# Optimization experiments

Hardware: AMD Instinct MI355X
Metric: run time of the kernel (lower is better)

## Reference

```python
import jax, jax.numpy as jnp
import numpy as np

B, N, DIM, H, DH = 16, 1024, 768, 12, 64
SCALE = DH ** -0.5


def setup_inputs() -> dict:
    key = jax.random.key(0)
    k1, k2, k3 = jax.random.split(key, 3)
    x = jax.random.normal(k1, (B, N, DIM), dtype=jnp.float32)
    W_qkv = jax.random.normal(k2, (DIM, 3 * H * DH), dtype=jnp.float32) * (DIM ** -0.5)
    W_out = jax.random.normal(k3, (H * DH, DIM), dtype=jnp.float32) * ((H * DH) ** -0.5)
    b_out = jnp.zeros((DIM,), dtype=jnp.float32)
    # perm = [0] + random shuffle of 1..N-1 (matches module's construction)
    rng = np.random.default_rng(0)
    perm = jnp.asarray(np.concatenate([[0], rng.permutation(np.arange(1, N))]), dtype=jnp.int32)
    return {"x": x, "W_qkv": W_qkv, "W_out": W_out, "b_out": b_out, "perm": perm}


def reference(x, W_qkv, W_out, b_out, perm):
    # QKV projection: [b, n, 3*h*d]
    qkv = jnp.einsum('bnd,de->bne', x, W_qkv)
    q, k, v = jnp.split(qkv, 3, axis=-1)
    # [b, n, h*d] -> [b, h, n, d]
    reshape = lambda t: t.reshape(B, N, H, DH).transpose(0, 2, 1, 3)
    q, k, v = reshape(q), reshape(k), reshape(v)
    # permute query rows
    q = q[:, :, perm]
    dots = jnp.einsum('bhqd,bhkd->bhqk', q, k) * SCALE
    attn = jax.nn.softmax(dots, axis=-1)
    out = jnp.einsum('bhqk,bhkd->bhqd', attn, v)
    out = out.transpose(0, 2, 1, 3).reshape(B, N, H * DH)
    return jnp.einsum('bne,ed->bnd', out, W_out) + b_out
```

## Files before the change

### kernel.cpp

```cpp
#include <hip/hip_runtime.h>
#include <hip/hip_bf16.h>


typedef __bf16 bf16x8 __attribute__((ext_vector_type(8)));
typedef __bf16 bf16x4 __attribute__((ext_vector_type(4)));
typedef float  f32x4  __attribute__((ext_vector_type(4)));

__device__ __forceinline__ f32x4 mfma16(bf16x8 a, bf16x8 b, f32x4 c) {
    return __builtin_amdgcn_mfma_f32_16x16x32_bf16(a, b, c, 0, 0, 0);
}

__device__ __forceinline__ void async16(const void* g, void* l) {
    __builtin_amdgcn_global_load_lds(
        (const __attribute__((address_space(1))) unsigned int*)g,
        (__attribute__((address_space(3))) unsigned int*)l,
        16, 0, 0);
}

__global__ void detect_dtype(const unsigned short* __restrict__ raw, int* __restrict__ flag) {
    __shared__ int cnt;
    if (threadIdx.x == 0) cnt = 0;
    __syncthreads();
    int local = 0;
    for (int i = threadIdx.x; i < 2048; i += 256) {
        unsigned e = (raw[i] >> 7) & 0xFFu;
        if (e >= 0xC0u) local++;
    }
    atomicAdd(&cnt, local);
    __syncthreads();
    if (threadIdx.x == 0) *flag = (cnt > 16) ? 1 : 0;
}

__global__ void convert_to_bf16(const void* __restrict__ src, __bf16* __restrict__ dst,
                                int n4, const int* __restrict__ flag) {
    const int f = *flag;
    int i = blockIdx.x * blockDim.x + threadIdx.x;
    const int stride = gridDim.x * blockDim.x;
    if (f) {
        const float4* s = (const float4*)src;
        for (; i < n4; i += stride) {
            float4 v = s[i];
            bf16x4 o;
            o[0] = (__bf16)v.x; o[1] = (__bf16)v.y;
            o[2] = (__bf16)v.z; o[3] = (__bf16)v.w;
            *(bf16x4*)&dst[(size_t)i * 4] = o;
        }
    } else {
        const ushort4* s = (const ushort4*)src;
        for (; i < n4; i += stride) *(ushort4*)&dst[(size_t)i * 4] = s[i];
    }
}

__global__ void transpose_dyn(const void* __restrict__ in, __bf16* __restrict__ out,
                              int R, int C, const int* __restrict__ flag) {
    __shared__ __bf16 tile[64][65];
    const int f = *flag;
    const int c0 = blockIdx.x * 64, r0 = blockIdx.y * 64;
    const int tx = threadIdx.x, ty = threadIdx.y;
#pragma unroll
    for (int k = 0; k < 16; ++k) {
        int r = ty + 4 * k;
        size_t idx = (size_t)(r0 + r) * C + c0 + tx;
        tile[r][tx] = f ? (__bf16)((const float*)in)[idx] : ((const __bf16*)in)[idx];
    }
    __syncthreads();
#pragma unroll
    for (int k = 0; k < 16; ++k) {
        int cc = ty + 4 * k;
        out[(size_t)(c0 + cc) * R + r0 + tx] = tile[tx][cc];
    }
}

__global__ void transpose_v(const __bf16* __restrict__ qkv, __bf16* __restrict__ vt) {
    __shared__ __bf16 tile[64][65];
    const int bh = blockIdx.y;
    const int b = bh / 12, h = bh % 12;
    const int n0 = blockIdx.x * 64;
    const int tx = threadIdx.x, ty = threadIdx.y;
#pragma unroll
    for (int k = 0; k < 16; ++k) {
        int n = ty + 4 * k;
        tile[n][tx] = qkv[((size_t)b * 1024 + n0 + n) * 2304 + 1536 + h * 64 + tx];
    }
    __syncthreads();
#pragma unroll
    for (int k = 0; k < 16; ++k) {
        int d = ty + 4 * k;
        vt[((size_t)bh * 64 + d) * 1024 + n0 + tx] = tile[tx][d];
    }
}

template <int MODE>
__global__ __launch_bounds__(256)
void gemm_bt(const __bf16* __restrict__ A, int lda,
             const __bf16* __restrict__ Bt,
             const void* __restrict__ bias,
             void* __restrict__ Cout, int ldc,
             int K, const int* __restrict__ flag) {
    __shared__ __align__(16) char smem[16384];
    __bf16* lsA = (__bf16*)smem;
    __bf16* lsB = (__bf16*)(smem + 8192);
    const int tid  = threadIdx.x;
    const int wid  = tid >> 6;
    const int lane = tid & 63;
    const int quad = lane >> 4;
    const int l15  = lane & 15;
    const int bm = blockIdx.x * 128;
    const int bn = blockIdx.y * 128;
    const int wm = (wid & 1) * 64;
    const int wn = (wid >> 1) * 64;
    const int srow  = lane >> 2;
    const int sslot = lane & 3;

    f32x4 acc[4][4];
#pragma unroll
    for (int i = 0; i < 4; ++i)
#pragma unroll
        for (int j = 0; j < 4; ++j) acc[i][j] = (f32x4)0.0f;

    for (int k0 = 0; k0 < K; k0 += 32) {
        __syncthreads();
#pragma unroll
        for (int is = 0; is < 2; ++is) {
            int r  = is * 64 + wid * 16 + srow;
            int gc = k0 + ((sslot ^ ((r >> 1) & 3)) << 3);
            async16(A + (size_t)(bm + r) * lda + gc, &lsA[(is * 64 + wid * 16) * 32]);
        }
#pragma unroll
        for (int is = 0; is < 2; ++is) {
            int r  = is * 64 + wid * 16 + srow;
            int gc = k0 + ((sslot ^ ((r >> 1) & 3)) << 3);
            async16(Bt + (size_t)(bn + r) * K + gc, &lsB[(is * 64 + wid * 16) * 32]);
        }
        __syncthreads();

        bf16x8 af[4], bfr[4];
#pragma unroll
        for (int mi = 0; mi < 4; ++mi) {
            int r = wm + mi * 16 + l15;
            af[mi] = *(const bf16x8*)&lsA[r * 32 + (quad ^ ((r >> 1) & 3)) * 8];
        }
#pragma unroll
        for (int ni = 0; ni < 4; ++ni) {
            int r = wn + ni * 16 + l15;
            bfr[ni] = *(const bf16x8*)&lsB[r * 32 + (quad ^ ((r >> 1) & 3)) * 8];
        }
#pragma unroll
        for (int mi = 0; mi < 4; ++mi)
#pragma unroll
            for (int ni = 0; ni < 4; ++ni)
                acc[mi][ni] = mfma16(af[mi], bfr[ni], acc[mi][ni]);
    }

    const int f = (MODE == 1) ? *flag : 0;
    if (MODE == 1) {
#pragma unroll
        for (int ni = 0; ni < 4; ++ni) {
            int col = bn + wn + ni * 16 + l15;
            float bv = f ? ((const float*)bias)[col] : (float)((const __bf16*)bias)[col];
#pragma unroll
            for (int mi = 0; mi < 4; ++mi)
#pragma unroll
                for (int rg = 0; rg < 4; ++rg) acc[mi][ni][rg] += bv;
        }
    }

    if (MODE == 0 || !f) {
        __bf16* cs = (__bf16*)smem;
#pragma unroll
        for (int c = 0; c < 4; ++c) {
            __syncthreads();
            if (wm == (c >> 1) * 64) {
                int mb = (c & 1) * 2;
#pragma unroll
                for (int mloc = 0; mloc < 2; ++mloc) {
                    int rowc = mloc * 16 + quad * 4;
#pragma unroll
                    for (int ni = 0; ni < 4; ++ni) {
                        int col = wn + ni * 16 + l15;
#pragma unroll
                        for (int rg = 0; rg < 4; ++rg)
                            cs[(rowc + rg) * 136 + col] = (__bf16)acc[mb + mloc][ni][rg];
                    }
                }
            }
            __syncthreads();
#pragma unroll
            for (int p = 0; p < 2; ++p) {
                int row  = p * 16 + (tid >> 4);
                int colc = tid & 15;
                bf16x8 v = *(const bf16x8*)&cs[row * 136 + colc * 8];
                *(bf16x8*)((__bf16*)Cout + (size_t)(bm + c * 32 + row) * ldc + bn + colc * 8) = v;
            }
        }
    } else {
        float* cs = (float*)smem;
#pragma unroll
        for (int c = 0; c < 8; ++c) {
            __syncthreads();
            if (wm == (c >> 2) * 64) {
                int mi = c & 3;
                int rowc = quad * 4;
#pragma unroll
                for (int ni = 0; ni < 4; ++ni) {
                    int col = wn + ni * 16 + l15;
#pragma unroll
                    for (int rg = 0; rg < 4; ++rg)
                        cs[(rowc + rg) * 132 + col] = acc[mi][ni][rg];
                }
            }
            __syncthreads();
#pragma unroll
            for (int p = 0; p < 2; ++p) {
                int row  = p * 8 + (tid >> 5);
                int colc = tid & 31;
                float4 v = *(const float4*)&cs[row * 132 + colc * 4];
                *(float4*)((float*)Cout + (size_t)(bm + c * 16 + row) * ldc + bn + colc * 4) = v;
            }
        }
    }
}

__global__ __launch_bounds__(256, 2)
void attn(const __bf16* qkv, const __bf16* __restrict__ vt,
          const int* __restrict__ perm, __bf16* O, int ldo) {
    __shared__ __align__(16) char smem[38912];
    __bf16* Qs = (__bf16*)smem;
    __bf16* Ks = (__bf16*)smem;
    __bf16* Vs = (__bf16*)(smem + 8192);
    __bf16* Ps = (__bf16*)(smem + 16384);

    const int tid  = threadIdx.x;
    const int wid  = tid >> 6;
    const int lane = tid & 63;
    const int quad = lane >> 4;
    const int l15  = lane & 15;
    const int bh = blockIdx.x;
    const int q0 = blockIdx.y * 128;
    const int b = bh / 12, h = bh % 12;
    const size_t row_base = (size_t)b * 1024;
    const int qcol = h * 64;
    const int kcol = 768 + h * 64;
    const int srow8  = lane >> 3;
    const int sslot8 = lane & 7;
    __bf16* Pw = Ps + wid * (32 * 88);

#pragma unroll
    for (int is = 0; is < 4; ++is) {
        int r = is * 32 + wid * 8 + srow8;
        int gr = perm[q0 + r];
        int chunk = sslot8 ^ (r & 7);
        async16(qkv + (row_base + gr) * 2304 + qcol + chunk * 8,
                &Qs[(is * 32 + wid * 8) * 64]);
    }
    __syncthreads();

    bf16x8 qf[2][2];
#pragma unroll
    for (int mi = 0; mi < 2; ++mi) {
        int r = wid * 32 + mi * 16 + l15;
#pragma unroll
        for (int ks = 0; ks < 2; ++ks)
            qf[mi][ks] = *(const bf16x8*)&Qs[r * 64 + (((ks * 4 + quad) ^ (r & 7)) * 8)];
    }

    const int off0 = l15 * 64 + (((0 * 4 + quad) ^ (l15 & 7)) * 8);
    const int off1 = l15 * 64 + (((1 * 4 + quad) ^ (l15 & 7)) * 8);
    const int pwb  = l15 * 88 + quad * 4;
    const int pfb  = l15 * 88 + quad * 8;

    const int rK = wid * 8 + srow8;
    const int ck = sslot8 ^ (rK & 7);
    const __bf16* kg0 = qkv + (row_base + rK) * 2304 + kcol + ck * 8;
    const __bf16* kg1 = kg0 + (size_t)32 * 2304;
    const __bf16* vg0 = vt + ((size_t)bh * 64 + rK) * 1024 + ck * 8;
    const __bf16* vg1 = vg0 + (size_t)32 * 1024;

    f32x4 acco[2][4];
#pragma unroll
    for (int mi = 0; mi < 2; ++mi)
#pragma unroll
        for (int ni = 0; ni < 4; ++ni) acco[mi][ni] = (f32x4)0.0f;
    float lsum[2] = {0.0f, 0.0f};

    const float cfac = 0.125f * 1.44269504088896340736f;

    for (int kt = 0; kt < 16; ++kt) {
        __syncthreads();
        async16(kg0, &Ks[(wid * 8) * 64]);
        async16(kg1, &Ks[(32 + wid * 8) * 64]);
        async16(vg0, &Vs[(wid * 8) * 64]);
        async16(vg1, &Vs[(32 + wid * 8) * 64]);
        kg0 += (size_t)64 * 2304;
        kg1 += (size_t)64 * 2304;
        vg0 += 64;
        vg1 += 64;
        __syncthreads();

#pragma unroll
        for (int half = 0; half < 2; ++half) {
            f32x4 accs[2][2];
#pragma unroll
            for (int ki = 0; ki < 2; ++ki)
#pragma unroll
                for (int mi = 0; mi < 2; ++mi) accs[ki][mi] = (f32x4)0.0f;
#pragma unroll
            for (int ks = 0; ks < 2; ++ks) {
                const int off = ks ? off1 : off0;
                bf16x8 kf0 = *(const bf16x8*)&Ks[(half * 2 + 0) * 1024 + off];
                bf16x8 kf1 = *(const bf16x8*)&Ks[(half * 2 + 1) * 1024 + off];
                accs[0][0] = mfma16(kf0, qf[0][ks], accs[0][0]);
                accs[0][1] = mfma16(kf0, qf[1][ks], accs[0][1]);
                accs[1][0] = mfma16(kf1, qf[0][ks], accs[1][0]);
                accs[1][1] = mfma16(kf1, qf[1][ks], accs[1][1]);
            }

#pragma unroll
            for (int ki = 0; ki < 2; ++ki)
#pragma unroll
                for (int mi = 0; mi < 2; ++mi) {
                    bf16x4 pk;
                    float s0 = __builtin_amdgcn_exp2f(accs[ki][mi][0] * cfac - 8.0f);
                    float s1 = __builtin_amdgcn_exp2f(accs[ki][mi][1] * cfac - 8.0f);
                    float s2 = __builtin_amdgcn_exp2f(accs[ki][mi][2] * cfac - 8.0f);
                    float s3 = __builtin_amdgcn_exp2f(accs[ki][mi][3] * cfac - 8.0f);
                    pk[0] = (__bf16)s0; pk[1] = (__bf16)s1;
                    pk[2] = (__bf16)s2; pk[3] = (__bf16)s3;
                    lsum[mi] += (s0 + s1) + (s2 + s3);
                    *(bf16x4*)&Pw[pwb + mi * 1408 + (half * 2 + ki) * 16] = pk;
                }

            {
                bf16x8 pf0 = *(const bf16x8*)&Pw[pfb + 0 * 1408 + half * 32];
                bf16x8 pf1 = *(const bf16x8*)&Pw[pfb + 1 * 1408 + half * 32];
                const int offv = half ? off1 : off0;
#pragma unroll
                for (int ni = 0; ni < 4; ++ni) {
                    bf16x8 vf = *(const bf16x8*)&Vs[ni * 1024 + offv];
                    acco[0][ni] = mfma16(pf0, vf, acco[0][ni]);
                    acco[1][ni] = mfma16(pf1, vf, acco[1][ni]);
                }
            }
        }
    }

#pragma unroll
    for (int off = 16; off < 64; off <<= 1) {
        lsum[0] += __shfl_xor(lsum[0], off, 64);
        lsum[1] += __shfl_xor(lsum[1], off, 64);
    }

#pragma unroll
    for (int mi = 0; mi < 2; ++mi) {
#pragma unroll
        for (int rg = 0; rg < 4; ++rg) {
            float inv = 1.0f / __shfl(lsum[mi], quad * 4 + rg, 64);
            int orow = q0 + wid * 32 + mi * 16 + quad * 4 + rg;
#pragma unroll
            for (int ni = 0; ni < 4; ++ni) {
                int ocol = h * 64 + ni * 16 + l15;
                O[(row_base + orow) * (size_t)ldo + ocol] = (__bf16)(acco[mi][ni][rg] * inv);
            }
        }
    }
}

extern "C" void kernel_launch(void* const* d_in, const int* in_sizes, int n_in,
                              void* d_out, int out_size, void* d_ws, size_t ws_size,
                              hipStream_t stream) {
    (void)in_sizes; (void)n_in; (void)out_size; (void)ws_size;
    const void* x_raw    = d_in[0];
    const void* Wqkv_raw = d_in[1];
    const void* Wout_raw = d_in[2];
    const void* bout_raw = d_in[3];
    const int*  perm     = (const int*)d_in[4];

    char* ws = (char*)d_ws;
    int*    flag = (int*)ws;
    __bf16* Xc   = (__bf16*)(ws + 256);
    __bf16* QKV  = (__bf16*)(ws + 25166080);
    __bf16* Vt   = (__bf16*)(ws + 100663552);
    __bf16* Wqt  = (__bf16*)(ws + 125829376);
    __bf16* Wot  = (__bf16*)(ws + 129368320);
    __bf16* Obuf = QKV + 1536;

    detect_dtype<<<1, 256, 0, stream>>>((const unsigned short*)x_raw, flag);
    convert_to_bf16<<<2048, 256, 0, stream>>>(x_raw, Xc, 16384 * 768 / 4, flag);
    transpose_dyn<<<dim3(36, 12), dim3(64, 4), 0, stream>>>(Wqkv_raw, Wqt, 768, 2304, flag);
    transpose_dyn<<<dim3(12, 12), dim3(64, 4), 0, stream>>>(Wout_raw, Wot, 768, 768, flag);
    gemm_bt<0><<<dim3(128, 18), 256, 0, stream>>>(Xc, 768, Wqt, nullptr, QKV, 2304, 768, nullptr);
    transpose_v<<<dim3(16, 192), dim3(64, 4), 0, stream>>>(QKV, Vt);
    attn<<<dim3(192, 8), 256, 0, stream>>>(QKV, Vt, perm, Obuf, 2304);
    gemm_bt<1><<<dim3(128, 6), 256, 0, stream>>>(Obuf, 2304, Wot, bout_raw, d_out, 768, 768, flag);
}
```

Measured before the change: 227.3 us.

## Use 256x256-tile double-buffered GEMM kernel for QKV projection

```diff
diff --git a/kernel.cpp b/kernel.cpp
--- a/kernel.cpp
+++ b/kernel.cpp
@@ -87,6 +87,181 @@
     for (int k = 0; k < 16; ++k) {
         int d = ty + 4 * k;
         vt[((size_t)bh * 64 + d) * 1024 + n0 + tx] = tile[tx][d];
+    }
+}
+
+__global__ __launch_bounds__(512, 2)
+void gemm256_bt(const __bf16* __restrict__ A, int lda,
+                const __bf16* __restrict__ Bt, int ldb,
+                __bf16* __restrict__ Cout, int ldc, int K) {
+    __shared__ __align__(16) char smem[131072];
+    const int tid  = threadIdx.x;
+    const int wid  = tid >> 6;
+    const int lane = tid & 63;
+    const int quad = lane >> 4;
+    const int l15  = lane & 15;
+    const int wr   = wid >> 2;
+    const int wc   = wid & 3;
+    const int bm = blockIdx.x * 256;
+    const int bn = blockIdx.y * 256;
+    const int srow8  = lane >> 3;
+    const int sslot8 = lane & 7;
+
+    const int offk[2] = { l15 * 128 + (((quad    ) ^ (l15 & 7)) * 16),
+                          l15 * 128 + (((quad | 4) ^ (l15 & 7)) * 16) };
+
+    const int cchunk = (sslot8 ^ srow8) * 8;
+    const __bf16* gA[4];
+    const __bf16* gB[4];
+#pragma unroll
+    for (int p = 0; p < 4; ++p) {
+        int r = (wid * 4 + p) * 8 + srow8;
+        gA[p] = A  + (size_t)(bm + r) * lda + cchunk;
+        gB[p] = Bt + (size_t)(bn + r) * ldb + cchunk;
+    }
+
+    f32x4 acc[8][4];
+#pragma unroll
+    for (int i = 0; i < 8; ++i)
+#pragma unroll
+        for (int j = 0; j < 4; ++j) acc[i][j] = (f32x4)0.0f;
+
+#pragma unroll
+    for (int p = 0; p < 4; ++p) {
+        async16(gA[p], smem + (wid * 4 + p) * 1024);
+        async16(gB[p], smem + 65536 + (wid * 4 + p) * 1024);
+        gA[p] += 64; gB[p] += 64;
+    }
+    asm volatile("s_waitcnt vmcnt(0)" ::: "memory");
+    __builtin_amdgcn_s_barrier();
+
+    const int nkt = K >> 6;
+    int cur = 0;
+#pragma unroll 1
+    for (int kt = 0; kt < nkt; ++kt) {
+        const bool notlast = (kt != nkt - 1);
+        const char* aRd = smem + cur + wr * 16384;
+        const char* bRd = smem + 65536 + cur + wc * 8192;
+        char* aSt = smem + (cur ^ 32768);
+        char* bSt = smem + 65536 + (cur ^ 32768);
+        bf16x8 af[4][2], bfr[4][2];
+
+#pragma unroll
+        for (int i = 0; i < 4; ++i)
+#pragma unroll
+            for (int kk = 0; kk < 2; ++kk)
+                af[i][kk] = *(const bf16x8*)(aRd + offk[kk] + i * 2048);
+#pragma unroll
+        for (int j = 0; j < 2; ++j)
+#pragma unroll
+            for (int kk = 0; kk < 2; ++kk)
+                bfr[j][kk] = *(const bf16x8*)(bRd + offk[kk] + j * 2048);
+        if (notlast) {
+#pragma unroll
+            for (int p = 0; p < 4; ++p) {
+                async16(gA[p], aSt + (wid * 4 + p) * 1024);
+                gA[p] += 64;
+            }
+        }
+        __builtin_amdgcn_s_barrier();
+        asm volatile("s_waitcnt lgkmcnt(0)" ::: "memory");
+        __builtin_amdgcn_sched_barrier(0);
+        __builtin_amdgcn_s_setprio(1);
+#pragma unroll
+        for (int i = 0; i < 4; ++i)
+#pragma unroll
+            for (int j = 0; j < 2; ++j)
+#pragma unroll
+                for (int kk = 0; kk < 2; ++kk)
+                    acc[i][j] = mfma16(af[i][kk], bfr[j][kk], acc[i][j]);
+        __builtin_amdgcn_s_setprio(0);
+        __builtin_amdgcn_s_barrier();
+
+#pragma unroll
+        for (int j = 0; j < 2; ++j)
+#pragma unroll
+            for (int kk = 0; kk < 2; ++kk)
+                bfr[2 + j][kk] = *(const bf16x8*)(bRd + offk[kk] + (2 + j) * 2048);
+        if (notlast) {
+#pragma unroll
+            for (int p = 0; p < 4; ++p) {
+                async16(gB[p], bSt + (wid * 4 + p) * 1024);
+                gB[p] += 64;
+            }
+        }
+        __builtin_amdgcn_s_barrier();
+        asm volatile("s_waitcnt lgkmcnt(0)" ::: "memory");
+        __builtin_amdgcn_sched_barrier(0);
+        __builtin_amdgcn_s_setprio(1);
+#pragma unroll
+        for (int i = 0; i < 4; ++i)
+#pragma unroll
+            for (int j = 0; j < 2; ++j)
+#pragma unroll
+                for (int kk = 0; kk < 2; ++kk)
+                    acc[i][2 + j] = mfma16(af[i][kk], bfr[2 + j][kk], acc[i][2 + j]);
+        __builtin_amdgcn_s_setprio(0);
+        __builtin_amdgcn_s_barrier();
+
+#pragma unroll
+        for (int i = 0; i < 4; ++i)
+#pragma unroll
+            for (int kk = 0; kk < 2; ++kk)
+                af[i][kk] = *(const bf16x8*)(aRd + offk[kk] + (4 + i) * 2048);
+        __builtin_amdgcn_s_barrier();
+        asm volatile("s_waitcnt lgkmcnt(0)" ::: "memory");
+        __builtin_amdgcn_sched_barrier(0);
+        __builtin_amdgcn_s_setprio(1);
+#pragma unroll
+        for (int i = 0; i < 4; ++i)
+#pragma unroll
+            for (int j = 0; j < 2; ++j)
+#pragma unroll
+                for (int kk = 0; kk < 2; ++kk)
+                    acc[4 + i][j] = mfma16(af[i][kk], bfr[j][kk], acc[4 + i][j]);
+        __builtin_amdgcn_s_setprio(0);
+        __builtin_amdgcn_s_barrier();
+
+        __builtin_amdgcn_s_setprio(1);
+#pragma unroll
+        for (int i = 0; i < 4; ++i)
+#pragma unroll
+            for (int j = 0; j < 2; ++j)
+#pragma unroll
+                for (int kk = 0; kk < 2; ++kk)
+                    acc[4 + i][2 + j] = mfma16(af[i][kk], bfr[2 + j][kk], acc[4 + i][2 + j]);
+        __builtin_amdgcn_s_setprio(0);
+        asm volatile("s_waitcnt vmcnt(0)" ::: "memory");
+        __builtin_amdgcn_s_barrier();
+        cur ^= 32768;
+    }
+
+    __bf16* cs = (__bf16*)smem;
+#pragma unroll 1
+    for (int c = 0; c < 8; ++c) {
+        __syncthreads();
+        if (wr == (c >> 2)) {
+            int mbase = (c & 3) * 2;
+#pragma unroll
+            for (int mloc = 0; mloc < 2; ++mloc) {
+#pragma unroll
+                for (int ni = 0; ni < 4; ++ni) {
+                    int col = wc * 64 + ni * 16 + l15;
+#pragma unroll
+                    for (int rg = 0; rg < 4; ++rg)
+                        cs[(mloc * 16 + quad * 4 + rg) * 264 + col] =
+                            (__bf16)acc[mbase + mloc][ni][rg];
+                }
+            }
+        }
+        __syncthreads();
+#pragma unroll
+        for (int p = 0; p < 2; ++p) {
+            int row  = p * 16 + (tid >> 5);
+            int colc = tid & 31;
+            bf16x8 v = *(const bf16x8*)&cs[row * 264 + colc * 8];
+            *(bf16x8*)&Cout[(size_t)(bm + c * 32 + row) * ldc + bn + colc * 8] = v;
+        }
     }
 }
 
@@ -388,7 +563,7 @@
     convert_to_bf16<<<2048, 256, 0, stream>>>(x_raw, Xc, 16384 * 768 / 4, flag);
     transpose_dyn<<<dim3(36, 12), dim3(64, 4), 0, stream>>>(Wqkv_raw, Wqt, 768, 2304, flag);
     transpose_dyn<<<dim3(12, 12), dim3(64, 4), 0, stream>>>(Wout_raw, Wot, 768, 768, flag);
-    gemm_bt<0><<<dim3(128, 18), 256, 0, stream>>>(Xc, 768, Wqt, nullptr, QKV, 2304, 768, nullptr);
+    gemm256_bt<<<dim3(64, 9), 512, 0, stream>>>(Xc, 768, Wqt, 768, QKV, 2304, 768);
     transpose_v<<<dim3(16, 192), dim3(64, 4), 0, stream>>>(QKV, Vt);
     attn<<<dim3(192, 8), 256, 0, stream>>>(QKV, Vt, perm, Obuf, 2304);
     gemm_bt<1><<<dim3(128, 6), 256, 0, stream>>>(Obuf, 2304, Wot, bout_raw, d_out, 768, 768, flag);
```

Result: slower. 308.4 us (+35.7%).

## Add 256x256 triple-buffered GEMM kernel for the QKV projection

Applied to the files above, without the earlier changes.

```diff
diff --git a/kernel.cpp b/kernel.cpp
--- a/kernel.cpp
+++ b/kernel.cpp
@@ -87,6 +87,132 @@
     for (int k = 0; k < 16; ++k) {
         int d = ty + 4 * k;
         vt[((size_t)bh * 64 + d) * 1024 + n0 + tx] = tile[tx][d];
+    }
+}
+
+#define MF4(I, AV) \
+    acc[I][0] = mfma16(AV, b0, acc[I][0]); \
+    acc[I][1] = mfma16(AV, b1, acc[I][1]); \
+    acc[I][2] = mfma16(AV, b2, acc[I][2]); \
+    acc[I][3] = mfma16(AV, b3, acc[I][3])
+
+#define TILE_STEP(RDOFF, STOFF, DO_STAGE, WAITKIND) do {                      \
+    const char* aRd = smem + (RDOFF) + wr * 8192;                             \
+    const char* bRd = smem + (RDOFF) + 16384 + wc * 4096;                     \
+    bf16x8 a0 = *(const bf16x8*)(aRd + laneoff + 0 * 1024);                   \
+    bf16x8 a1 = *(const bf16x8*)(aRd + laneoff + 1 * 1024);                   \
+    bf16x8 a2 = *(const bf16x8*)(aRd + laneoff + 2 * 1024);                   \
+    bf16x8 a3 = *(const bf16x8*)(aRd + laneoff + 3 * 1024);                   \
+    bf16x8 b0 = *(const bf16x8*)(bRd + laneoff + 0 * 1024);                   \
+    bf16x8 b1 = *(const bf16x8*)(bRd + laneoff + 1 * 1024);                   \
+    bf16x8 b2 = *(const bf16x8*)(bRd + laneoff + 2 * 1024);                   \
+    bf16x8 b3 = *(const bf16x8*)(bRd + laneoff + 3 * 1024);                   \
+    if (DO_STAGE) {                                                           \
+        char* stA = smem + (STOFF) + wid * 2048;                              \
+        async16(gA0, stA); async16(gA1, stA + 1024);                          \
+        gA0 += 32; gA1 += 32;                                                 \
+    }                                                                         \
+    __builtin_amdgcn_s_setprio(1);                                            \
+    MF4(0, a0); MF4(1, a1); MF4(2, a2); MF4(3, a3);                           \
+    __builtin_amdgcn_s_setprio(0);                                            \
+    bf16x8 a4 = *(const bf16x8*)(aRd + laneoff + 4 * 1024);                   \
+    bf16x8 a5 = *(const bf16x8*)(aRd + laneoff + 5 * 1024);                   \
+    bf16x8 a6 = *(const bf16x8*)(aRd + laneoff + 6 * 1024);                   \
+    bf16x8 a7 = *(const bf16x8*)(aRd + laneoff + 7 * 1024);                   \
+    if (DO_STAGE) {                                                           \
+        char* stB = smem + (STOFF) + 16384 + wid * 2048;                      \
+        async16(gB0, stB); async16(gB1, stB + 1024);                          \
+        gB0 += 32; gB1 += 32;                                                 \
+    }                                                                         \
+    __builtin_amdgcn_s_setprio(1);                                            \
+    MF4(4, a4); MF4(5, a5); MF4(6, a6); MF4(7, a7);                           \
+    __builtin_amdgcn_s_setprio(0);                                            \
+    if ((WAITKIND) == 1)      asm volatile("s_waitcnt vmcnt(4)" ::: "memory");\
+    else if ((WAITKIND) == 0) asm volatile("s_waitcnt vmcnt(0)" ::: "memory");\
+    if ((WAITKIND) >= 0) __builtin_amdgcn_s_barrier();                        \
+} while (0)
+
+__global__ __launch_bounds__(512, 2)
+void gemm256_bt(const __bf16* __restrict__ A, int lda,
+                const __bf16* __restrict__ Bt, int ldb,
+                __bf16* __restrict__ Cout, int ldc, int K) {
+    __shared__ __align__(16) char smem[98304];
+    const int tid  = threadIdx.x;
+    const int wid  = tid >> 6;
+    const int lane = tid & 63;
+    const int quad = lane >> 4;
+    const int l15  = lane & 15;
+    const int wr   = wid >> 2;
+    const int wc   = wid & 3;
+    const int bm = blockIdx.x * 256;
+    const int bn = blockIdx.y * 256;
+
+    const int laneoff = l15 * 64 + ((quad ^ (l15 & 3)) * 16);
+
+    const int srow  = lane >> 2;
+    const int cchunk = (((lane & 3) ^ (srow & 3))) * 8;
+    const __bf16* gA0 = A  + (size_t)(bm + wid * 32 + srow) * lda + cchunk;
+    const __bf16* gA1 = gA0 + (size_t)16 * lda;
+    const __bf16* gB0 = Bt + (size_t)(bn + wid * 32 + srow) * ldb + cchunk;
+    const __bf16* gB1 = gB0 + (size_t)16 * ldb;
+
+    f32x4 acc[8][4];
+#pragma unroll
+    for (int i = 0; i < 8; ++i)
+#pragma unroll
+        for (int j = 0; j < 4; ++j) acc[i][j] = (f32x4)0.0f;
+
+    {
+        char* st = smem + wid * 2048;
+        async16(gA0, st); async16(gA1, st + 1024); gA0 += 32; gA1 += 32;
+        st = smem + 16384 + wid * 2048;
+        async16(gB0, st); async16(gB1, st + 1024); gB0 += 32; gB1 += 32;
+        st = smem + 32768 + wid * 2048;
+        async16(gA0, st); async16(gA1, st + 1024); gA0 += 32; gA1 += 32;
+        st = smem + 49152 + wid * 2048;
+        async16(gB0, st); async16(gB1, st + 1024); gB0 += 32; gB1 += 32;
+    }
+    asm volatile("s_waitcnt vmcnt(4)" ::: "memory");
+    __builtin_amdgcn_s_barrier();
+
+    const int n3 = (K >> 5) / 3 - 1;
+#pragma unroll 1
+    for (int kt3 = 0; kt3 < n3; ++kt3) {
+        TILE_STEP(0,     65536, 1, 1);
+        TILE_STEP(32768, 0,     1, 1);
+        TILE_STEP(65536, 32768, 1, 1);
+    }
+    TILE_STEP(0,     65536, 1, 1);
+    TILE_STEP(32768, 0,     0, 0);
+    TILE_STEP(65536, 0,     0, -1);
+#undef TILE_STEP
+#undef MF4
+
+    __bf16* cs = (__bf16*)smem;
+#pragma unroll
+    for (int c = 0; c < 8; ++c) {
+        __syncthreads();
+        if (wr == (c >> 2)) {
+#pragma unroll
+            for (int mloc = 0; mloc < 2; ++mloc) {
+#pragma unroll
+                for (int ni = 0; ni < 4; ++ni) {
+                    int col = wc * 64 + ni * 16 + l15;
+#pragma unroll
+                    for (int rg = 0; rg < 4; ++rg)
+                        cs[(mloc * 16 + quad * 4 + rg) * 264 + col] =
+                            (__bf16)acc[(c & 3) * 2 + mloc][ni][rg];
+                }
+            }
+        }
+        __syncthreads();
+#pragma unroll
+        for (int p = 0; p < 2; ++p) {
+            int row  = p * 16 + (tid >> 5);
+            int colc = tid & 31;
+            bf16x8 v = *(const bf16x8*)&cs[row * 264 + colc * 8];
+            *(bf16x8*)&Cout[(size_t)(bm + c * 32 + row) * ldc + bn + colc * 8] = v;
+        }
     }
 }
 
@@ -388,7 +514,7 @@
     convert_to_bf16<<<2048, 256, 0, stream>>>(x_raw, Xc, 16384 * 768 / 4, flag);
     transpose_dyn<<<dim3(36, 12), dim3(64, 4), 0, stream>>>(Wqkv_raw, Wqt, 768, 2304, flag);
     transpose_dyn<<<dim3(12, 12), dim3(64, 4), 0, stream>>>(Wout_raw, Wot, 768, 768, flag);
-    gemm_bt<0><<<dim3(128, 18), 256, 0, stream>>>(Xc, 768, Wqt, nullptr, QKV, 2304, 768, nullptr);
+    gemm256_bt<<<dim3(64, 9), 512, 0, stream>>>(Xc, 768, Wqt, 768, QKV, 2304, 768);
     transpose_v<<<dim3(16, 192), dim3(64, 4), 0, stream>>>(QKV, Vt);
     attn<<<dim3(192, 8), 256, 0, stream>>>(QKV, Vt, perm, Obuf, 2304);
     gemm_bt<1><<<dim3(128, 6), 256, 0, stream>>>(Obuf, 2304, Wot, bout_raw, d_out, 768, 768, flag);
```

Result: no change. 231.8 us (+1.9%).

## Double-buffer GEMM LDS tiles with async prefetch and swizzle block order

Applied to the files above, without the earlier changes.

```diff
diff --git a/kernel.cpp b/kernel.cpp
--- a/kernel.cpp
+++ b/kernel.cpp
@@ -90,66 +90,114 @@
     }
 }
 
+#define GMFMA16()                                                       \
+    acc[0][0] = mfma16(af0, bf0, acc[0][0]);                            \
+    acc[0][1] = mfma16(af0, bf1, acc[0][1]);                            \
+    acc[0][2] = mfma16(af0, bf2, acc[0][2]);                            \
+    acc[0][3] = mfma16(af0, bf3, acc[0][3]);                            \
+    acc[1][0] = mfma16(af1, bf0, acc[1][0]);                            \
+    acc[1][1] = mfma16(af1, bf1, acc[1][1]);                            \
+    acc[1][2] = mfma16(af1, bf2, acc[1][2]);                            \
+    acc[1][3] = mfma16(af1, bf3, acc[1][3]);                            \
+    acc[2][0] = mfma16(af2, bf0, acc[2][0]);                            \
+    acc[2][1] = mfma16(af2, bf1, acc[2][1]);                            \
+    acc[2][2] = mfma16(af2, bf2, acc[2][2]);                            \
+    acc[2][3] = mfma16(af2, bf3, acc[2][3]);                            \
+    acc[3][0] = mfma16(af3, bf0, acc[3][0]);                            \
+    acc[3][1] = mfma16(af3, bf1, acc[3][1]);                            \
+    acc[3][2] = mfma16(af3, bf2, acc[3][2]);                            \
+    acc[3][3] = mfma16(af3, bf3, acc[3][3])
+
+#define GTILE(RD, ST, DO_STAGE, DO_SYNC) do {                           \
+    if (DO_STAGE) {                                                     \
+        async16(gA0, smem + (ST) + stA0);                               \
+        async16(gA1, smem + (ST) + stA1);                               \
+        async16(gB0, smem + (ST) + 8192 + stA0);                        \
+        async16(gB1, smem + (ST) + 8192 + stA1);                        \
+        gA0 += 32; gA1 += 32; gB0 += 32; gB1 += 32;                     \
+    }                                                                   \
+    bf16x8 af0 = *(const bf16x8*)(smem + (RD) + aoff0);                 \
+    bf16x8 af1 = *(const bf16x8*)(smem + (RD) + aoff1);                 \
+    bf16x8 af2 = *(const bf16x8*)(smem + (RD) + aoff2);                 \
+    bf16x8 af3 = *(const bf16x8*)(smem + (RD) + aoff3);                 \
+    bf16x8 bf0 = *(const bf16x8*)(smem + (RD) + boff0);                 \
+    bf16x8 bf1 = *(const bf16x8*)(smem + (RD) + boff1);                 \
+    bf16x8 bf2 = *(const bf16x8*)(smem + (RD) + boff2);                 \
+    bf16x8 bf3 = *(const bf16x8*)(smem + (RD) + boff3);                 \
+    GMFMA16();                                                          \
+    if (DO_SYNC) {                                                      \
+        asm volatile("s_waitcnt vmcnt(0)" ::: "memory");                \
+        __builtin_amdgcn_s_barrier();                                   \
+    }                                                                   \
+} while (0)
+
 template <int MODE>
-__global__ __launch_bounds__(256)
+__global__ __launch_bounds__(256, 3)
 void gemm_bt(const __bf16* __restrict__ A, int lda,
              const __bf16* __restrict__ Bt,
              const void* __restrict__ bias,
              void* __restrict__ Cout, int ldc,
              int K, const int* __restrict__ flag) {
-    __shared__ __align__(16) char smem[16384];
-    __bf16* lsA = (__bf16*)smem;
-    __bf16* lsB = (__bf16*)(smem + 8192);
+    __shared__ __align__(16) char smem[32768];
     const int tid  = threadIdx.x;
     const int wid  = tid >> 6;
     const int lane = tid & 63;
     const int quad = lane >> 4;
     const int l15  = lane & 15;
-    const int bm = blockIdx.x * 128;
-    const int bn = blockIdx.y * 128;
+
+    const int nwg = gridDim.x * gridDim.y;
+    const int bid = blockIdx.x + gridDim.x * blockIdx.y;
+    const int swz = (bid & 7) * (nwg >> 3) + (bid >> 3);
+    const int bm = (swz % gridDim.x) * 128;
+    const int bn = (swz / gridDim.x) * 128;
+
     const int wm = (wid & 1) * 64;
     const int wn = (wid >> 1) * 64;
     const int srow  = lane >> 2;
     const int sslot = lane & 3;
 
+    const int rA0 = wid * 16 + srow;
+    const int rA1 = 64 + wid * 16 + srow;
+    const __bf16* gA0 = A  + (size_t)(bm + rA0) * lda + ((sslot ^ ((rA0 >> 1) & 3)) << 3);
+    const __bf16* gA1 = A  + (size_t)(bm + rA1) * lda + ((sslot ^ ((rA1 >> 1) & 3)) << 3);
+    const __bf16* gB0 = Bt + (size_t)(bn + rA0) * K   + ((sslot ^ ((rA0 >> 1) & 3)) << 3);
+    const __bf16* gB1 = Bt + (size_t)(bn + rA1) * K   + ((sslot ^ ((rA1 >> 1) & 3)) << 3);
+    const int stA0 = (wid * 16) * 64;
+    const int stA1 = (64 + wid * 16) * 64;
+
+    const int rf0 = wm + 0 * 16 + l15, rf1 = wm + 1 * 16 + l15;
+    const int rf2 = wm + 2 * 16 + l15, rf3 = wm + 3 * 16 + l15;
+    const int aoff0 = rf0 * 64 + ((quad ^ ((rf0 >> 1) & 3)) * 16);
+    const int aoff1 = rf1 * 64 + ((quad ^ ((rf1 >> 1) & 3)) * 16);
+    const int aoff2 = rf2 * 64 + ((quad ^ ((rf2 >> 1) & 3)) * 16);
+    const int aoff3 = rf3 * 64 + ((quad ^ ((rf3 >> 1) & 3)) * 16);
+    const int rg0 = wn + 0 * 16 + l15, rg1 = wn + 1 * 16 + l15;
+    const int rg2 = wn + 2 * 16 + l15, rg3 = wn + 3 * 16 + l15;
+    const int boff0 = 8192 + rg0 * 64 + ((quad ^ ((rg0 >> 1) & 3)) * 16);
+    const int boff1 = 8192 + rg1 * 64 + ((quad ^ ((rg1 >> 1) & 3)) * 16);
+    const int boff2 = 8192 + rg2 * 64 + ((quad ^ ((rg2 >> 1) & 3)) * 16);
+    const int boff3 = 8192 + rg3 * 64 + ((quad ^ ((rg3 >> 1) & 3)) * 16);
+
     f32x4 acc[4][4];
 #pragma unroll
     for (int i = 0; i < 4; ++i)
 #pragma unroll
         for (int j = 0; j < 4; ++j) acc[i][j] = (f32x4)0.0f;
 
-    for (int k0 = 0; k0 < K; k0 += 32) {
-        __syncthreads();
-#pragma unroll
-        for (int is = 0; is < 2; ++is) {
-            int r  = is * 64 + wid * 16 + srow;
-            int gc = k0 + ((sslot ^ ((r >> 1) & 3)) << 3);
-            async16(A + (size_t)(bm + r) * lda + gc, &lsA[(is * 64 + wid * 16) * 32]);
-        }
-#pragma unroll
-        for (int is = 0; is < 2; ++is) {
-            int r  = is * 64 + wid * 16 + srow;
-            int gc = k0 + ((sslot ^ ((r >> 1) & 3)) << 3);
-            async16(Bt + (size_t)(bn + r) * K + gc, &lsB[(is * 64 + wid * 16) * 32]);
-        }
-        __syncthreads();
-
-        bf16x8 af[4], bfr[4];
-#pragma unroll
-        for (int mi = 0; mi < 4; ++mi) {
-            int r = wm + mi * 16 + l15;
-            af[mi] = *(const bf16x8*)&lsA[r * 32 + (quad ^ ((r >> 1) & 3)) * 8];
-        }
-#pragma unroll
-        for (int ni = 0; ni < 4; ++ni) {
-            int r = wn + ni * 16 + l15;
-            bfr[ni] = *(const bf16x8*)&lsB[r * 32 + (quad ^ ((r >> 1) & 3)) * 8];
-        }
-#pragma unroll
-        for (int mi = 0; mi < 4; ++mi)
-#pragma unroll
-            for (int ni = 0; ni < 4; ++ni)
-                acc[mi][ni] = mfma16(af[mi], bfr[ni], acc[mi][ni]);
+    async16(gA0, smem + stA0);
+    async16(gA1, smem + stA1);
+    async16(gB0, smem + 8192 + stA0);
+    async16(gB1, smem + 8192 + stA1);
+    gA0 += 32; gA1 += 32; gB0 += 32; gB1 += 32;
+    asm volatile("s_waitcnt vmcnt(0)" ::: "memory");
+    __builtin_amdgcn_s_barrier();
+
+    const int nkt = K >> 5;
+#pragma unroll 1
+    for (int kt = 0; kt < nkt; kt += 2) {
+        const bool more = (kt + 2 < nkt);
+        GTILE(0,     16384, true, true);
+        GTILE(16384, 0,     more, more);
     }
 
     const int f = (MODE == 1) ? *flag : 0;
```

Measured after the change: 232.6 us. 2.3% more time.
